# Kernel tuning notes

Hardware: AMD Instinct MI355X
Metric: run time of the kernel (lower is better)

## Reference

```python
import jax, jax.numpy as jnp
import numpy as np

STRIDE, PAD, DIL = 1, 1, 1
EPS = 1e-12
RHO_LIM = 1.0 - 1e-6
PI = jnp.pi


def clamp_pg(x, lo=0.0):
    # clamp value but pass gradient through (clamp_preserve_grad)
    return x + jax.lax.stop_gradient(jnp.maximum(x, lo) - x)


def setup_inputs() -> dict:
    key = jax.random.key(0)
    B, N, T, K = 8, 128, 1024, 3
    k = jax.random.uniform(key, (B, B, N, T, 2), dtype=jnp.float32)
    leak = jnp.array(1.0, dtype=jnp.float32)
    alpha = jnp.full((1, 1, K), 1.0 / K, dtype=jnp.float32)
    beta = jnp.array(0.0, dtype=jnp.float32)
    return {"k": k, "leak": leak, "alpha": alpha, "beta": beta}


def reference(k, leak, alpha, beta):
    k_gp, k_ntk = k[..., 0], k[..., 1]          # (B,B,N,T) each
    B, _, N, T = k_gp.shape

    # v[b,t] = k_gp[b,b,0,t]  (diagonal over batch dims, first lag)
    ar = jnp.arange(B)
    v = k_gp[ar, ar, 0, :]                      # (B,T)
    v_pad = jnp.pad(v, ((0, 0), (0, N - 1)))    # (B, T+N-1)

    v_xx = v[:, None, None, :]                  # (B,1,1,T)
    idx = jnp.arange(N)[:, None] + jnp.arange(T)[None, :]  # (N,T)
    v_yy = v_pad[:, idx][None]                  # (1,B,N,T): v_pad[b, n+t]

    # calculate_statistics
    std_x = jnp.sqrt(jnp.maximum(v_xx, 0.0))
    std_y = jnp.sqrt(jnp.maximum(v_yy, 0.0))
    denom = jnp.maximum(std_x * std_y, EPS)
    rho = jnp.clip(k_gp / denom, -RHO_LIM, RHO_LIM)  # (B,B,N,T)

    a = clamp_pg(leak)
    theta = jnp.arccos(rho)
    s = jnp.sqrt(1.0 - rho * rho)
    one_m = (1.0 - a) ** 2
    coef = 1.0 + a * a
    # leaky-ReLU arccos kernel and its derivative kernel
    c0 = std_x * std_y / (2.0 * PI) * (one_m * s + rho * (coef * PI - one_m * theta))
    c1 = (coef * PI - one_m * theta) / (2.0 * PI)

    w = clamp_pg(alpha)                         # (1,1,K)

    def conv(x):  # x: (B,B,N,T) -> (B,B,N,T')
        y = jax.lax.conv_general_dilated(
            x.reshape(-1, 1, T), w, window_strides=(STRIDE,),
            padding=[(PAD, PAD)], rhs_dilation=(DIL,),
            dimension_numbers=("NCH", "OIH", "NCH"))
        return y.reshape(B, B, N, -1)

    kg = conv(c0)
    kn = conv(c1 * k_ntk) + kg

    b = clamp_pg(beta)
    kg = kg + b
    kn = kn + b
    return jnp.stack([kg, kn], axis=-1)
```

## Files before the change

kernel.cpp:

```cpp
#include <hip/hip_runtime.h>
#include <math.h>

#define BDIM 8
#define NDIM 128
#define TDIM 1024
#define TPB 256

#define EPS_F 1e-12f
#define RHO_LIM_F (1.0f - 1e-6f)
#define PI_F 3.14159265358979323846f


__device__ __forceinline__ void kfun(float kgp, float kntk, float vx, float vy,
                                     float one_m, float coef, bool fast,
                                     float& c0, float& cn)
{
    const float inv2pi = 0.15915494309189535f;
    const float p = sqrtf(fmaxf(vx, 0.0f) * fmaxf(vy, 0.0f));
    const float r = fminf(fmaxf(kgp * __builtin_amdgcn_rcpf(fmaxf(p, EPS_F)), -RHO_LIM_F), RHO_LIM_F);
    if (fast) {
        const float hc = 0.5f * coef;
        c0 = p * r * hc;
        cn = hc * kntk;
    } else {
        const float th = acosf(r);
        const float s  = sqrtf(1.0f - r * r);
        const float br = coef * PI_F - one_m * th;
        c0 = p * inv2pi * (one_m * s + r * br);
        cn = br * inv2pi * kntk;
    }
}

__global__ __launch_bounds__(TPB) void conv_arccos_kernel(
    const float* __restrict__ k,
    const float* __restrict__ leak,
    const float* __restrict__ alpha,
    const float* __restrict__ beta,
    float* __restrict__ out)
{
    const int row  = blockIdx.x;
    const int n    = row % NDIM;
    const int bb   = row / NDIM;
    const int b2   = bb % BDIM;
    const int b1   = bb / BDIM;
    const int tid  = threadIdx.x;
    const int lane = tid & 63;

    const float a   = fmaxf(leak[0], 0.0f);
    const float w0  = fmaxf(alpha[0], 0.0f);
    const float w1  = fmaxf(alpha[1], 0.0f);
    const float w2  = fmaxf(alpha[2], 0.0f);
    const float bia = fmaxf(beta[0], 0.0f);

    const float one_m = (1.0f - a) * (1.0f - a);
    const float coef  = 1.0f + a * a;
    const bool  fast  = (one_m == 0.0f);

    const float4* krow4 = (const float4*)(k + (size_t)row * TDIM * 2);
    const float2* krow2 = (const float2*)(k + (size_t)row * TDIM * 2);
    const float2* vrx = (const float2*)(k) + (size_t)(b1 * BDIM + b1) * NDIM * TDIM;
    const float2* vry = (const float2*)(k) + (size_t)(b2 * BDIM + b2) * NDIM * TDIM;
    float4* orow = (float4*)(out + (size_t)row * TDIM * 2);

    const int lim = TDIM - n;

    #pragma unroll
    for (int j = 0; j < TDIM / (2 * TPB); ++j) {
        const int f = tid + j * TPB;
        const int t = 2 * f;

        const float4 kv  = krow4[f];
        const float4 vx2 = ((const float4*)vrx)[f];
        const float vy0 = (t     < lim) ? vry[n + t    ].x : 0.0f;
        const float vy1 = (t + 1 < lim) ? vry[n + t + 1].x : 0.0f;

        float c00, cn0, c01, cn1;
        kfun(kv.x, kv.y, vx2.x, vy0, one_m, coef, fast, c00, cn0);
        kfun(kv.z, kv.w, vx2.z, vy1, one_m, coef, fast, c01, cn1);

        float c0l = __shfl_up(c01, 1);
        float cnl = __shfl_up(cn1, 1);
        float c0r = __shfl_down(c00, 1);
        float cnr = __shfl_down(cn0, 1);

        const bool lo = (lane == 0);
        const bool hi = (lane == 63);
        if (lo || hi) {
            const int e = lo ? (t - 1) : (t + 2);
            float ec0 = 0.0f, ecn = 0.0f;
            if (e >= 0 && e < TDIM) {
                const float2 kp  = krow2[e];
                const float  evx = vrx[e].x;
                const float  evy = (e < lim) ? vry[n + e].x : 0.0f;
                kfun(kp.x, kp.y, evx, evy, one_m, coef, fast, ec0, ecn);
            }
            if (lo) { c0l = ec0; cnl = ecn; }
            else    { c0r = ec0; cnr = ecn; }
        }

        const float kg0 = w0 * c0l + w1 * c00 + w2 * c01;
        const float kg1 = w0 * c00 + w1 * c01 + w2 * c0r;
        const float kn0 = w0 * cnl + w1 * cn0 + w2 * cn1 + kg0;
        const float kn1 = w0 * cn0 + w1 * cn1 + w2 * cnr + kg1;

        float4 o;
        o.x = kg0 + bia;
        o.y = kn0 + bia;
        o.z = kg1 + bia;
        o.w = kn1 + bia;
        orow[f] = o;
    }
}

extern "C" void kernel_launch(void* const* d_in, const int* in_sizes, int n_in,
                              void* d_out, int out_size, void* d_ws, size_t ws_size,
                              hipStream_t stream) {
    const float* k     = (const float*)d_in[0];
    const float* leak  = (const float*)d_in[1];
    const float* alpha = (const float*)d_in[2];
    const float* beta  = (const float*)d_in[3];
    float* out = (float*)d_out;

    const int n_rows = BDIM * BDIM * NDIM;
    conv_arccos_kernel<<<n_rows, TPB, 0, stream>>>(k, leak, alpha, beta, out);
}
```

Before: 128.6 us.

## Process four lag rows per block with LDS halo exchange and shared v loads

Each 512-thread block now handles four consecutive lag rows. The diagonal vx and vy vectors are loaded once and reused across those rows, with vy shifted by one element per row. The 3-tap conv neighbours are exchanged through shared memory with zeroed halo slots, replacing the wave shuffles and the extra edge-lane recompute. The fast path drops the reciprocal and clamps kgp directly against p*RHO_LIM, and bias is folded into FMAs. The costs are a block-wide barrier and extra LDS traffic.

```diff
diff --git a/kernel.cpp b/kernel.cpp
--- a/kernel.cpp
+++ b/kernel.cpp
@@ -4,7 +4,9 @@
 #define BDIM 8
 #define NDIM 128
 #define TDIM 1024
-#define TPB 256
+#define TPB 512
+#define ROWS 4
+#define LSTRIDE 1028
 
 #define EPS_F 1e-12f
 #define RHO_LIM_F (1.0f - 1e-6f)
@@ -17,12 +19,13 @@
 {
     const float inv2pi = 0.15915494309189535f;
     const float p = sqrtf(fmaxf(vx, 0.0f) * fmaxf(vy, 0.0f));
-    const float r = fminf(fmaxf(kgp * __builtin_amdgcn_rcpf(fmaxf(p, EPS_F)), -RHO_LIM_F), RHO_LIM_F);
     if (fast) {
         const float hc = 0.5f * coef;
-        c0 = p * r * hc;
+        const float pr = p * RHO_LIM_F;
+        c0 = hc * fminf(fmaxf(kgp, -pr), pr);
         cn = hc * kntk;
     } else {
+        const float r  = fminf(fmaxf(kgp * __builtin_amdgcn_rcpf(fmaxf(p, EPS_F)), -RHO_LIM_F), RHO_LIM_F);
         const float th = acosf(r);
         const float s  = sqrtf(1.0f - r * r);
         const float br = coef * PI_F - one_m * th;
@@ -38,13 +41,16 @@
     const float* __restrict__ beta,
     float* __restrict__ out)
 {
-    const int row  = blockIdx.x;
-    const int n    = row % NDIM;
-    const int bb   = row / NDIM;
+    __shared__ float sc0[ROWS * LSTRIDE];
+    __shared__ float scn[ROWS * LSTRIDE];
+
+    const int base = blockIdx.x * ROWS;
+    const int n0   = base % NDIM;
+    const int bb   = base / NDIM;
     const int b2   = bb % BDIM;
     const int b1   = bb / BDIM;
     const int tid  = threadIdx.x;
-    const int lane = tid & 63;
+    const int t    = tid * 2;
 
     const float a   = fmaxf(leak[0], 0.0f);
     const float w0  = fmaxf(alpha[0], 0.0f);
@@ -56,59 +62,59 @@
     const float coef  = 1.0f + a * a;
     const bool  fast  = (one_m == 0.0f);
 
-    const float4* krow4 = (const float4*)(k + (size_t)row * TDIM * 2);
-    const float2* krow2 = (const float2*)(k + (size_t)row * TDIM * 2);
     const float2* vrx = (const float2*)(k) + (size_t)(b1 * BDIM + b1) * NDIM * TDIM;
     const float2* vry = (const float2*)(k) + (size_t)(b2 * BDIM + b2) * NDIM * TDIM;
-    float4* orow = (float4*)(out + (size_t)row * TDIM * 2);
 
-    const int lim = TDIM - n;
+    if (tid < ROWS * 2) {
+        const int r   = tid >> 1;
+        const int idx = r * LSTRIDE + ((tid & 1) ? (TDIM + 1) : 0);
+        sc0[idx] = 0.0f;
+        scn[idx] = 0.0f;
+    }
+
+    const float4 vx2 = ((const float4*)vrx)[tid];
+    const float4* vyp = (const float4*)(vry + (n0 + t));
+    const float4 vyA = vyp[0];
+    const float4 vyB = vyp[1];
+    float y0 = vyA.x, y1 = vyA.z, y2 = vyB.x, y3 = vyB.z;
+    float y4 = vry[n0 + t + 4].x;
+    const int ty = n0 + t;
+    if (ty     >= TDIM) y0 = 0.0f;
+    if (ty + 1 >= TDIM) y1 = 0.0f;
+    if (ty + 2 >= TDIM) y2 = 0.0f;
+    if (ty + 3 >= TDIM) y3 = 0.0f;
+    if (ty + 4 >= TDIM) y4 = 0.0f;
+    const float yv[6] = { y0, y1, y2, y3, y4, 0.0f };
 
     #pragma unroll
-    for (int j = 0; j < TDIM / (2 * TPB); ++j) {
-        const int f = tid + j * TPB;
-        const int t = 2 * f;
+    for (int rl = 0; rl < ROWS; ++rl) {
+        const float4 kv = ((const float4*)(k + (size_t)(base + rl) * TDIM * 2))[tid];
+        float c00, cn0, c01, cn1;
+        kfun(kv.x, kv.y, vx2.x, yv[rl],     one_m, coef, fast, c00, cn0);
+        kfun(kv.z, kv.w, vx2.z, yv[rl + 1], one_m, coef, fast, c01, cn1);
+        const int bi = rl * LSTRIDE + t + 1;
+        sc0[bi]     = c00;
+        sc0[bi + 1] = c01;
+        scn[bi]     = cn0;
+        scn[bi + 1] = cn1;
+    }
 
-        const float4 kv  = krow4[f];
-        const float4 vx2 = ((const float4*)vrx)[f];
-        const float vy0 = (t     < lim) ? vry[n + t    ].x : 0.0f;
-        const float vy1 = (t + 1 < lim) ? vry[n + t + 1].x : 0.0f;
+    __syncthreads();
 
-        float c00, cn0, c01, cn1;
-        kfun(kv.x, kv.y, vx2.x, vy0, one_m, coef, fast, c00, cn0);
-        kfun(kv.z, kv.w, vx2.z, vy1, one_m, coef, fast, c01, cn1);
+    #pragma unroll
+    for (int rl = 0; rl < ROWS; ++rl) {
+        const int bi = rl * LSTRIDE + t;
+        const float c0l = sc0[bi], c00 = sc0[bi + 1], c01 = sc0[bi + 2], c0r = sc0[bi + 3];
+        const float cnl = scn[bi], cn0 = scn[bi + 1], cn1 = scn[bi + 2], cnr = scn[bi + 3];
 
-        float c0l = __shfl_up(c01, 1);
-        float cnl = __shfl_up(cn1, 1);
-        float c0r = __shfl_down(c00, 1);
-        float cnr = __shfl_down(cn0, 1);
-
-        const bool lo = (lane == 0);
-        const bool hi = (lane == 63);
-        if (lo || hi) {
-            const int e = lo ? (t - 1) : (t + 2);
-            float ec0 = 0.0f, ecn = 0.0f;
-            if (e >= 0 && e < TDIM) {
-                const float2 kp  = krow2[e];
-                const float  evx = vrx[e].x;
-                const float  evy = (e < lim) ? vry[n + e].x : 0.0f;
-                kfun(kp.x, kp.y, evx, evy, one_m, coef, fast, ec0, ecn);
-            }
-            if (lo) { c0l = ec0; cnl = ecn; }
-            else    { c0r = ec0; cnr = ecn; }
-        }
-
-        const float kg0 = w0 * c0l + w1 * c00 + w2 * c01;
-        const float kg1 = w0 * c00 + w1 * c01 + w2 * c0r;
-        const float kn0 = w0 * cnl + w1 * cn0 + w2 * cn1 + kg0;
-        const float kn1 = w0 * cn0 + w1 * cn1 + w2 * cnr + kg1;
+        const float kg0 = fmaf(w0, c0l, fmaf(w1, c00, fmaf(w2, c01, bia)));
+        const float kg1 = fmaf(w0, c00, fmaf(w1, c01, fmaf(w2, c0r, bia)));
+        const float kn0 = fmaf(w0, cnl, fmaf(w1, cn0, fmaf(w2, cn1, kg0)));
+        const float kn1 = fmaf(w0, cn0, fmaf(w1, cn1, fmaf(w2, cnr, kg1)));
 
         float4 o;
-        o.x = kg0 + bia;
-        o.y = kn0 + bia;
-        o.z = kg1 + bia;
-        o.w = kn1 + bia;
-        orow[f] = o;
+        o.x = kg0; o.y = kn0; o.z = kg1; o.w = kn1;
+        ((float4*)(out + (size_t)(base + rl) * TDIM * 2))[tid] = o;
     }
 }
 
@@ -121,6 +127,6 @@
     const float* beta  = (const float*)d_in[3];
     float* out = (float*)d_out;
 
-    const int n_rows = BDIM * BDIM * NDIM;
-    conv_arccos_kernel<<<n_rows, TPB, 0, stream>>>(k, leak, alpha, beta, out);
+    const int n_blocks = BDIM * BDIM * NDIM / ROWS;
+    conv_arccos_kernel<<<n_blocks, TPB, 0, stream>>>(k, leak, alpha, beta, out);
 }
```

Result: faster. 119.8 us (-6.8%).
